# Kernel tuning notes

Hardware: AMD Instinct MI355X
Metric: run time of the kernel (lower is better)

## Reference

```python
import jax, jax.numpy as jnp
import numpy as np

B, T, N, D = 32, 64, 300, 128


def setup_inputs() -> dict:
    key = jax.random.key(0)
    k1, k2, k3, k4 = jax.random.split(key, 4)
    src = jax.random.normal(k1, (B, T, N, D), dtype=jnp.float32)
    # Parameters are zeros-initialized in the original module (untrained);
    # use small random values so the reference computes nontrivial math.
    wt1 = jax.random.normal(k2, (D,), dtype=jnp.float32) * 0.1
    wt2 = jax.random.normal(k3, (N, D), dtype=jnp.float32) * 0.1
    wt3 = jax.random.normal(k4, (N,), dtype=jnp.float32) * 0.1
    return {"src": src, "wt1": wt1, "wt2": wt2, "wt3": wt3}


def reference(src, wt1, wt2, wt3):
    # src: [B, T, N, D]
    Q = jnp.einsum('btnd,d->btn', src, wt1)            # [B, T, N]
    K = jnp.einsum('n,btnd->btd', wt3, src)            # [B, T, D]
    # bilinear score: Q @ wt2 @ K^T per batch -> [B, T, T]
    scores = jnp.einsum('bqn,nd,bkd->bqk', Q, wt2, K)
    # NOTE: original applies softmax over dim=0 (the batch axis) — faithful here.
    att = jax.nn.softmax(scores, axis=0)               # [B, Tq, Tk]
    # time-mixing: 'btnd,bta->band' -> output indexed [b, a(=T), n, d]
    mixed = jnp.einsum('btnd,bta->band', src, att)     # [B, T, N, D]
    return src + mixed  # dropout = identity at eval
```

## Files before the change

kernel.cpp:

```cpp
#include <hip/hip_runtime.h>

#define Bb 32
#define Tt 64
#define Nn 300
#define Dd 128
#define NC (Nn * Dd)
#define BTND ((size_t)Tt * NC)

__global__ __launch_bounds__(256) void qk_kernel(
        const float* __restrict__ src, const float* __restrict__ wt1,
        const float* __restrict__ wt3, float* __restrict__ Q,
        float* __restrict__ K) {
    __shared__ float wt3_s[Nn];
    __shared__ float kred[4 * Dd];
    const int tid = threadIdx.x;
    const int wave = tid >> 6, lane = tid & 63;
    for (int i = tid; i < Nn; i += 256) wt3_s[i] = wt3[i];
    __syncthreads();
    const int d0 = lane * 2;
    const float2 w1 = *(const float2*)(wt1 + d0);
    const float* sbt = src + (size_t)blockIdx.x * NC;
    float* Qrow = Q + (size_t)blockIdx.x * Nn;
    float kx = 0.f, ky = 0.f;
    for (int n = wave; n < Nn; n += 4) {
        float2 v = *(const float2*)(sbt + n * Dd + d0);
        float q = v.x * w1.x + v.y * w1.y;
        #pragma unroll
        for (int off = 32; off > 0; off >>= 1) q += __shfl_down(q, off, 64);
        if (lane == 0) Qrow[n] = q;
        float w3 = wt3_s[n];
        kx = fmaf(w3, v.x, kx);
        ky = fmaf(w3, v.y, ky);
    }
    kred[wave * Dd + d0] = kx;
    kred[wave * Dd + d0 + 1] = ky;
    __syncthreads();
    if (tid < Dd) {
        float s = kred[tid] + kred[Dd + tid] + kred[2 * Dd + tid] + kred[3 * Dd + tid];
        K[(size_t)blockIdx.x * Dd + tid] = s;
    }
}

__global__ __launch_bounds__(128) void score_kernel(
        const float* __restrict__ Q, const float* __restrict__ K,
        const float* __restrict__ wt2, float* __restrict__ scores) {
    __shared__ float qs[Nn];
    __shared__ float qws[Dd];
    const int tid = threadIdx.x;
    const int bq = blockIdx.x;
    const float* Qrow = Q + (size_t)bq * Nn;
    for (int i = tid; i < Nn; i += 128) qs[i] = Qrow[i];
    __syncthreads();
    float qw = 0.f;
    for (int n = 0; n < Nn; ++n) qw = fmaf(qs[n], wt2[n * Dd + tid], qw);
    qws[tid] = qw;
    __syncthreads();
    if (tid < Tt) {
        const int b = bq >> 6;
        const float* Krow = K + (size_t)(b * Tt + tid) * Dd;
        float s = 0.f;
        for (int d = 0; d < Dd; ++d) s = fmaf(qws[d], Krow[d], s);
        scores[(size_t)bq * Tt + tid] = s;
    }
}

__global__ __launch_bounds__(256) void softmax_b_kernel(
        const float* __restrict__ scores, float* __restrict__ att) {
    const int idx = blockIdx.x * 256 + threadIdx.x;
    float v[Bb];
    float m = -1e30f;
    #pragma unroll
    for (int b = 0; b < Bb; ++b) {
        v[b] = scores[b * (Tt * Tt) + idx];
        m = fmaxf(m, v[b]);
    }
    float sum = 0.f;
    #pragma unroll
    for (int b = 0; b < Bb; ++b) {
        float e = __expf(v[b] - m);
        v[b] = e;
        sum += e;
    }
    const float inv = 1.0f / sum;
    #pragma unroll
    for (int b = 0; b < Bb; ++b) att[b * (Tt * Tt) + idx] = v[b] * inv;
}

__global__ __launch_bounds__(256, 4) void mix_kernel(
        const float* __restrict__ src, const float* __restrict__ att,
        float* __restrict__ out) {
    __shared__ float att_s[Tt * Tt];
    const int tid = threadIdx.x;
    const int b = blockIdx.y;
    for (int i = tid; i < Tt * Tt; i += 256) {
        int t = i >> 6, a = i & 63;
        float v = att[(size_t)b * Tt * Tt + i];
        att_s[i] = v + (t == a ? 1.0f : 0.0f);
    }
    __syncthreads();
    const int j = blockIdx.x * 256 + tid;
    const float* sb = src + (size_t)b * BTND + j;
    float* ob = out + (size_t)b * BTND + j;
    float acc[Tt];
    #pragma unroll
    for (int a = 0; a < Tt; ++a) acc[a] = 0.f;
    float x = sb[0];
    for (int t = 0; t < Tt; ++t) {
        float xn = 0.f;
        if (t < Tt - 1) xn = sb[(size_t)(t + 1) * NC];
        const float* arow = att_s + t * Tt;
        #pragma unroll
        for (int a = 0; a < Tt; ++a) acc[a] = fmaf(arow[a], x, acc[a]);
        x = xn;
    }
    #pragma unroll
    for (int a = 0; a < Tt; ++a) ob[(size_t)a * NC] = acc[a];
}

extern "C" void kernel_launch(void* const* d_in, const int* in_sizes, int n_in,
                              void* d_out, int out_size, void* d_ws, size_t ws_size,
                              hipStream_t stream) {
    const float* src = (const float*)d_in[0];
    const float* wt1 = (const float*)d_in[1];
    const float* wt2 = (const float*)d_in[2];
    const float* wt3 = (const float*)d_in[3];
    float* out = (float*)d_out;

    float* ws = (float*)d_ws;
    float* Q      = ws;
    float* K      = Q + (size_t)Bb * Tt * Nn;
    float* scores = K + (size_t)Bb * Tt * Dd;
    float* att    = scores + (size_t)Bb * Tt * Tt;

    qk_kernel<<<Bb * Tt, 256, 0, stream>>>(src, wt1, wt3, Q, K);
    score_kernel<<<Bb * Tt, 128, 0, stream>>>(Q, K, wt2, scores);
    softmax_b_kernel<<<(Tt * Tt) / 256, 256, 0, stream>>>(scores, att);
    dim3 g4(NC / 256, Bb);
    mix_kernel<<<g4, 256, 0, stream>>>(src, att, out);
}
```

Before: 747.6 us.

## Split mix output rows across waves and vectorize column access with float4

Each block now handles 256 columns with 64 lanes doing float4 loads, and the four waves each own 16 of the 64 output time rows rather than every thread owning all 64. Loads and stores become 128-bit and the per-FMA shared-memory weight reads are amortised over four columns. In exchange, each wave re-reads the same src tile from global memory (4x redundant loads, likely served by cache), and the per-thread register footprint stays at 64 accumulators.

```diff
diff --git a/kernel.cpp b/kernel.cpp
--- a/kernel.cpp
+++ b/kernel.cpp
@@ -98,23 +98,37 @@
         att_s[i] = v + (t == a ? 1.0f : 0.0f);
     }
     __syncthreads();
-    const int j = blockIdx.x * 256 + tid;
+    const int lane = tid & 63;
+    const int ag = tid >> 6;
+    const int j = blockIdx.x * 256 + lane * 4;
     const float* sb = src + (size_t)b * BTND + j;
     float* ob = out + (size_t)b * BTND + j;
-    float acc[Tt];
+
+    float4 acc[16];
     #pragma unroll
-    for (int a = 0; a < Tt; ++a) acc[a] = 0.f;
-    float x = sb[0];
+    for (int i = 0; i < 16; ++i) acc[i] = make_float4(0.f, 0.f, 0.f, 0.f);
+
+    float4 x = *(const float4*)(sb);
     for (int t = 0; t < Tt; ++t) {
-        float xn = 0.f;
-        if (t < Tt - 1) xn = sb[(size_t)(t + 1) * NC];
-        const float* arow = att_s + t * Tt;
+        float4 xn = make_float4(0.f, 0.f, 0.f, 0.f);
+        if (t < Tt - 1) xn = *(const float4*)(sb + (size_t)(t + 1) * NC);
+        const float4* arow = (const float4*)(att_s + t * Tt + ag * 16);
+        float4 w0 = arow[0], w1 = arow[1], w2 = arow[2], w3 = arow[3];
+        const float wv[16] = {w0.x, w0.y, w0.z, w0.w, w1.x, w1.y, w1.z, w1.w,
+                              w2.x, w2.y, w2.z, w2.w, w3.x, w3.y, w3.z, w3.w};
         #pragma unroll
-        for (int a = 0; a < Tt; ++a) acc[a] = fmaf(arow[a], x, acc[a]);
+        for (int i = 0; i < 16; ++i) {
+            acc[i].x = fmaf(wv[i], x.x, acc[i].x);
+            acc[i].y = fmaf(wv[i], x.y, acc[i].y);
+            acc[i].z = fmaf(wv[i], x.z, acc[i].z);
+            acc[i].w = fmaf(wv[i], x.w, acc[i].w);
+        }
         x = xn;
     }
     #pragma unroll
-    for (int a = 0; a < Tt; ++a) ob[(size_t)a * NC] = acc[a];
+    for (int i = 0; i < 16; ++i) {
+        *(float4*)(ob + (size_t)(ag * 16 + i) * NC) = acc[i];
+    }
 }
 
 extern "C" void kernel_launch(void* const* d_in, const int* in_sizes, int n_in,
```

Result: slower. 1.373 ms (+83.7%).
